# Optimization experiments

Measured on AMD Instinct MI355X. Metric: run time of the kernel, lower is better.

The kernel has to match this reference:

```python
import jax, jax.numpy as jnp
import numpy as np

M_BIT = 8      # BfpConfig.bfp_M_Bit (sign + mantissa bits)
BLOCK = 64     # BFP block size along contraction (K) dim
K_SIZE, STRIDE, PAD = 3, 1, 1


def bfp_quantize(x, m_bit=M_BIT, block=BLOCK):
    """Block-floating-point quantize along last axis: per-block shared exponent
    from max-abs, m_bit-wide signed mantissa, then dequantize back to fp."""
    shape = x.shape
    xb = x.reshape(shape[:-1] + (shape[-1] // block, block))
    maxabs = jnp.max(jnp.abs(xb), axis=-1, keepdims=True)
    exp = jnp.floor(jnp.log2(jnp.maximum(maxabs, jnp.float32(1e-38))))
    scale = jnp.exp2(exp - (m_bit - 2))          # lsb weight for this block
    qmax = jnp.float32(2.0 ** (m_bit - 1) - 1)
    q = jnp.clip(jnp.round(xb / scale), -qmax - 1.0, qmax) * scale
    q = jnp.where(maxabs == 0.0, 0.0, q)
    return q.reshape(shape)


def im2col(x, k, s, p):
    """Torch Unfold ordering: columns flattened as (C, kh, kw). x: [N,C,H,W]."""
    N, C, H, W = x.shape
    Ho = (H + 2 * p - k) // s + 1
    Wo = (W + 2 * p - k) // s + 1
    xp = jnp.pad(x, ((0, 0), (0, 0), (p, p), (p, p)))
    rows = []
    for i in range(k):
        for j in range(k):
            rows.append(xp[:, :, i:i + s * Ho:s, j:j + s * Wo:s])  # [N,C,Ho,Wo]
    # [k*k, N, C, Ho, Wo] -> [N, C, k*k, Ho*Wo] -> [N, C*k*k, Ho*Wo]
    patches = jnp.stack(rows, axis=0).transpose(1, 2, 0, 3, 4)
    return patches.reshape(N, C * k * k, Ho * Wo), Ho, Wo


def setup_inputs() -> dict:
    key = jax.random.key(0)
    k1, k2, k3 = jax.random.split(key, 3)
    inputs = jax.random.normal(k1, (32, 128, 56, 56), dtype=jnp.float32)
    fan_in = 128 * K_SIZE * K_SIZE
    weight = jax.random.normal(k2, (256, 128, K_SIZE, K_SIZE), dtype=jnp.float32) / np.sqrt(fan_in)
    bias = jax.random.normal(k3, (256,), dtype=jnp.float32) * 0.01
    return {"inputs": inputs, "weight": weight, "bias": bias}


def reference(inputs, weight, bias):
    N = inputs.shape[0]
    C_out = weight.shape[0]
    cols, Ho, Wo = im2col(inputs, K_SIZE, STRIDE, PAD)      # [N, K, Ho*Wo]
    a = cols.transpose(0, 2, 1).reshape(-1, cols.shape[1])  # [N*Ho*Wo, K]
    w = weight.reshape(C_out, -1)                           # [C_out, K]
    qa = bfp_quantize(a)
    qw = bfp_quantize(w)
    out = qa @ qw.T + bias                                  # [N*Ho*Wo, C_out]
    out = out.reshape(N, Ho, Wo, C_out).transpose(0, 3, 1, 2)
    return out
```

## Files before the change

### kernel.cpp

```cpp
#include <hip/hip_runtime.h>

typedef short short8 __attribute__((ext_vector_type(8)));
typedef __bf16 bf16x8 __attribute__((ext_vector_type(8)));
typedef float floatx4 __attribute__((ext_vector_type(4)));

__device__ __forceinline__ float make_pow2(int e) {
  return __builtin_bit_cast(float, (unsigned)((e + 127) << 23));
}

typedef __attribute__((address_space(3))) void lds_void;
typedef const __attribute__((address_space(1))) void glob_void;
__device__ __forceinline__ void gload_lds16(const void* g, void* l) {
  __builtin_amdgcn_global_load_lds((glob_void*)g, (lds_void*)l, 16, 0, 0);
}

__global__ void quant_w_kernel(const float* __restrict__ w, unsigned short* __restrict__ qw) {
  int b = blockIdx.x;
  int row = b / 18, kb = b - row * 18;
  int t = threadIdx.x;
  int idx = row * 1152 + kb * 64 + t;
  float v = w[idx];
  float a = fabsf(v);
  #pragma unroll
  for (int off = 32; off; off >>= 1) a = fmaxf(a, __shfl_xor(a, off));
  float q = 0.f;
  if (a > 0.f) {
    int e = (int)((__builtin_bit_cast(unsigned, a) >> 23) & 0xffu) - 127;
    if (e < -126) e = -126;
    float inv = make_pow2(6 - e);
    float s   = make_pow2(e - 6);
    float r = rintf(v * inv);
    r = fminf(fmaxf(r, -128.f), 127.f);
    q = r * s;
  }
  qw[idx] = (unsigned short)(__builtin_bit_cast(unsigned, q) >> 16);
}

__global__ __launch_bounds__(512, 4) void conv_bfp_kernel(
    const float* __restrict__ in, const unsigned short* __restrict__ qw,
    const float* __restrict__ bias, float* __restrict__ out) {
  __shared__ unsigned short As[64 * 64];
  __shared__ unsigned short Bs[2][256 * 64];
  __shared__ float pmax[2][8][64];

  const int bid = blockIdx.x;
  const int mt = (bid & 7) * 196 + (bid >> 3);
  const int t = threadIdx.x;
  const int lane = t & 63;
  const int wave = __builtin_amdgcn_readfirstlane(t >> 6);

  const unsigned m = mt * 64u + lane;
  const unsigned nimg = m / 3136u;
  const unsigned py = m - nimg * 3136u;
  const int y = (int)(py / 56u);
  const int x = (int)(py - (unsigned)y * 56u);
  const int vbase = (int)((nimg * 401408u + (unsigned)y * 56u + (unsigned)x) * 4u);
  int vm = 0;
  #pragma unroll
  for (int i = 0; i < 3; ++i)
    #pragma unroll
    for (int j = 0; j < 3; ++j)
      if ((unsigned)(y + i - 1) < 56u && (unsigned)(x + j - 1) < 56u)
        vm |= 1 << (i * 3 + j);

  const int l3 = lane >> 3, l7 = lane & 7;
  const char* bsrc = (const char*)qw + (size_t)((wave * 32 + l3) * 2304) + ((l7 ^ l3) * 16);

  const int lr = lane & 15;
  const int lk = (lane >> 4) << 4;
  const int swz = (lr & 7) << 4;

  floatx4 acc[4][2] = {};

  auto gather = [&](float (&av)[8], int kb) {
    const int k0 = __builtin_amdgcn_readfirstlane(kb * 64 + wave * 8);
    #pragma unroll
    for (int u = 0; u < 8; ++u) {
      int k = k0 + u;
      int c = (int)((unsigned)k / 9u);
      int ij = k - c * 9;
      int soff = c * 3136 + (ij / 3) * 56 + (ij % 3) - 57;
      const char* pk = (const char*)in + (ptrdiff_t)soff * 4;
      float v = 0.f;
      if ((vm >> ij) & 1)
        v = *(const float*)(pk + vbase);
      av[u] = v;
    }
  };

  auto stage = [&](int kb) {
    char* bdst = (char*)Bs[kb & 1] + wave * 4096;
    #pragma unroll
    for (int c8 = 0; c8 < 4; ++c8)
      gload_lds16(bsrc + (size_t)c8 * 18432 + kb * 128, bdst + c8 * 1024);
  };

  auto lmax_store = [&](float (&av)[8], int kb) {
    float lm = 0.f;
    #pragma unroll
    for (int u = 0; u < 8; ++u) lm = fmaxf(lm, fabsf(av[u]));
    pmax[kb & 1][wave][lane] = lm;
  };

  auto quantWrite = [&](float (&av)[8], int kb) {
    const float* pb = &pmax[kb & 1][0][lane];
    float ma = 0.f;
    #pragma unroll
    for (int j = 0; j < 8; ++j) ma = fmaxf(ma, pb[j * 64]);
    short8 aq;
    if (ma > 0.f) {
      int e = (int)((__builtin_bit_cast(unsigned, ma) >> 23) & 0xffu) - 127;
      if (e < -126) e = -126;
      float inv = make_pow2(6 - e);
      float s   = make_pow2(e - 6);
      #pragma unroll
      for (int u = 0; u < 8; ++u) {
        float r = rintf(av[u] * inv);
        r = fminf(fmaxf(r, -128.f), 127.f);
        float q = r * s;
        aq[u] = (short)(unsigned short)(__builtin_bit_cast(unsigned, q) >> 16);
      }
    } else {
      aq = (short8)0;
    }
    char* arow = (char*)As + lane * 128;
    *(short8*)(arow + ((wave * 16) ^ ((lane & 7) << 4))) = aq;
  };

  float av0[8], av1[8];

  stage(0);
  gather(av0, 0);
  lmax_store(av0, 0);
  __syncthreads();
  quantWrite(av0, 0);
  gather(av1, 1);
  lmax_store(av1, 1);
  __syncthreads();

  auto phase = [&](int kb, float (&avq)[8], float (&avg)[8]) {
    bf16x8 afr[2][4];
    #pragma unroll
    for (int ks = 0; ks < 2; ++ks)
      #pragma unroll
      for (int f = 0; f < 4; ++f)
        afr[ks][f] = __builtin_bit_cast(bf16x8,
            *(const short8*)((const char*)As + (f * 16 + lr) * 128 + ((ks * 64 + lk) ^ swz)));
    __syncthreads();

    if (kb < 17) {
      quantWrite(avq, kb + 1);
      stage(kb + 1);
    }
    if (kb < 16) gather(avg, kb + 2);

    const char* bbase = (const char*)Bs[kb & 1];
    #pragma unroll
    for (int ks = 0; ks < 2; ++ks) {
      const int kbyte = (ks * 64 + lk) ^ swz;
      bf16x8 bfr[2];
      #pragma unroll
      for (int f = 0; f < 2; ++f)
        bfr[f] = __builtin_bit_cast(bf16x8,
            *(const short8*)(bbase + (wave * 32 + f * 16 + lr) * 128 + kbyte));
      #pragma unroll
      for (int fm = 0; fm < 4; ++fm)
        #pragma unroll
        for (int fn = 0; fn < 2; ++fn)
          acc[fm][fn] = __builtin_amdgcn_mfma_f32_16x16x32_bf16(bfr[fn], afr[ks][fm], acc[fm][fn], 0, 0, 0);
    }

    if (kb < 16) lmax_store(avg, kb + 2);
    if (kb < 17) __syncthreads();
  };

  #pragma unroll 1
  for (int kb = 0; kb < 18; kb += 2) {
    phase(kb, av1, av0);
    phase(kb + 1, av0, av1);
  }

  const unsigned ni = (mt * 64u) / 3136u;
  const unsigned pp0 = mt * 64u - ni * 3136u;
  float* obase = out + (size_t)ni * 802816u + pp0;
  const int cg = (lane >> 4) << 2;
  #pragma unroll
  for (int fn = 0; fn < 2; ++fn) {
    floatx4 bv = *(const floatx4*)&bias[wave * 32 + fn * 16 + cg];
    #pragma unroll
    for (int r = 0; r < 4; ++r) {
      int co = wave * 32 + fn * 16 + cg + r;
      float* orow = obase + (size_t)co * 3136u;
      #pragma unroll
      for (int fm = 0; fm < 4; ++fm)
        orow[fm * 16 + lr] = acc[fm][fn][r] + bv[r];
    }
  }
}

extern "C" void kernel_launch(void* const* d_in, const int* in_sizes, int n_in,
                              void* d_out, int out_size, void* d_ws, size_t ws_size,
                              hipStream_t stream) {
  const float* in   = (const float*)d_in[0];
  const float* w    = (const float*)d_in[1];
  const float* bias = (const float*)d_in[2];
  float* out = (float*)d_out;
  unsigned short* qw = (unsigned short*)d_ws;

  quant_w_kernel<<<4608, 64, 0, stream>>>(w, qw);
  conv_bfp_kernel<<<1568, 512, 0, stream>>>(in, qw, bias, out);
}
```

Before: 137.5 us.

## Deepen activation gather pipeline to three stages with explicit waitcnt barriers

Extends the software pipeline so global activation gathers are issued two K-blocks ahead using three rotating register buffers. __syncthreads is replaced with a custom barrier that waits only on LDS counters, and partial vmcnt waits let gathers stay in flight across MFMA blocks. MFMA sections are also raised in wave priority. The aim is to hide global-load latency behind compute, at the cost of more registers, which may lower occupancy, and hand-tuned vmcnt counts that must match the issued loads exactly.

```diff
diff --git a/kernel.cpp b/kernel.cpp
--- a/kernel.cpp
+++ b/kernel.cpp
@@ -12,6 +12,19 @@
 typedef const __attribute__((address_space(1))) void glob_void;
 __device__ __forceinline__ void gload_lds16(const void* g, void* l) {
   __builtin_amdgcn_global_load_lds((glob_void*)g, (lds_void*)l, 16, 0, 0);
+}
+
+__device__ __forceinline__ void barrier_lgkm() {
+  asm volatile("s_waitcnt lgkmcnt(0)" ::: "memory");
+  __builtin_amdgcn_sched_barrier(0);
+  __builtin_amdgcn_s_barrier();
+  asm volatile("" ::: "memory");
+  __builtin_amdgcn_sched_barrier(0);
+}
+
+template <int N> __device__ __forceinline__ void wait_vmcnt() {
+  asm volatile("s_waitcnt vmcnt(%0)" :: "n"(N) : "memory");
+  __builtin_amdgcn_sched_barrier(0);
 }
 
 __global__ void quant_w_kernel(const float* __restrict__ w, unsigned short* __restrict__ qw) {
@@ -127,34 +140,18 @@
     *(short8*)(arow + ((wave * 16) ^ ((lane & 7) << 4))) = aq;
   };
 
-  float av0[8], av1[8];
-
-  stage(0);
-  gather(av0, 0);
-  lmax_store(av0, 0);
-  __syncthreads();
-  quantWrite(av0, 0);
-  gather(av1, 1);
-  lmax_store(av1, 1);
-  __syncthreads();
-
-  auto phase = [&](int kb, float (&avq)[8], float (&avg)[8]) {
-    bf16x8 afr[2][4];
+  auto preloadA = [&](bf16x8 (&afr)[2][4]) {
     #pragma unroll
     for (int ks = 0; ks < 2; ++ks)
       #pragma unroll
       for (int f = 0; f < 4; ++f)
         afr[ks][f] = __builtin_bit_cast(bf16x8,
             *(const short8*)((const char*)As + (f * 16 + lr) * 128 + ((ks * 64 + lk) ^ swz)));
-    __syncthreads();
-
-    if (kb < 17) {
-      quantWrite(avq, kb + 1);
-      stage(kb + 1);
-    }
-    if (kb < 16) gather(avg, kb + 2);
-
+  };
+
+  auto mfmaBlk = [&](bf16x8 (&afr)[2][4], int kb) {
     const char* bbase = (const char*)Bs[kb & 1];
+    __builtin_amdgcn_s_setprio(1);
     #pragma unroll
     for (int ks = 0; ks < 2; ++ks) {
       const int kbyte = (ks * 64 + lk) ^ swz;
@@ -169,15 +166,67 @@
         for (int fn = 0; fn < 2; ++fn)
           acc[fm][fn] = __builtin_amdgcn_mfma_f32_16x16x32_bf16(bfr[fn], afr[ks][fm], acc[fm][fn], 0, 0, 0);
     }
-
-    if (kb < 16) lmax_store(avg, kb + 2);
-    if (kb < 17) __syncthreads();
+    __builtin_amdgcn_s_setprio(0);
+  };
+
+  float avA[8], avB[8], avC[8];
+
+  stage(0);
+  gather(avA, 0);
+  gather(avB, 1);
+  lmax_store(avA, 0);
+  barrier_lgkm();
+  quantWrite(avA, 0);
+  gather(avC, 2);
+  lmax_store(avB, 1);
+  barrier_lgkm();
+
+  auto phase = [&](int kb, float (&q)[8], float (&l)[8], float (&g)[8]) {
+    bf16x8 afr[2][4];
+    preloadA(afr);
+    barrier_lgkm();
+    quantWrite(q, kb + 1);
+    stage(kb + 1);
+    gather(g, kb + 3);
+    wait_vmcnt<20>();
+    mfmaBlk(afr, kb);
+    lmax_store(l, kb + 2);
+    barrier_lgkm();
   };
 
   #pragma unroll 1
-  for (int kb = 0; kb < 18; kb += 2) {
-    phase(kb, av1, av0);
-    phase(kb + 1, av0, av1);
+  for (int kb = 0; kb < 15; kb += 3) {
+    phase(kb,     avB, avC, avA);
+    phase(kb + 1, avC, avA, avB);
+    phase(kb + 2, avA, avB, avC);
+  }
+
+  {
+    bf16x8 afr[2][4];
+    preloadA(afr);
+    barrier_lgkm();
+    quantWrite(avB, 16);
+    stage(16);
+    wait_vmcnt<12>();
+    mfmaBlk(afr, 15);
+    lmax_store(avC, 17);
+    barrier_lgkm();
+  }
+  {
+    bf16x8 afr[2][4];
+    preloadA(afr);
+    barrier_lgkm();
+    quantWrite(avC, 17);
+    stage(17);
+    wait_vmcnt<4>();
+    mfmaBlk(afr, 16);
+    barrier_lgkm();
+  }
+  {
+    bf16x8 afr[2][4];
+    preloadA(afr);
+    wait_vmcnt<0>();
+    mfmaBlk(afr, 17);
   }
 
   const unsigned ni = (mt * 64u) / 3136u;
```

Result: no change. 139.2 us (+1.2%).

## Pre-swizzle quantized weights into MFMA fragment layout and load B directly to registers

Applied to the files above, without the earlier changes.

The weight quantizer now writes bf16 weights in a per-16-channel, per-k-block fragment order so each lane can load its MFMA B operand with one 16-byte global load. This removes the B shared-memory tile and its async global-to-LDS staging. The A tile is double-buffered instead, so each phase needs one barrier rather than two. The MFMA block runs at raised priority with A fragments read from LDS inside the loop. The cost is that B now comes through the global/L2 path into registers, and more registers are held by the double-buffered B fragments.

```diff
diff --git a/kernel.cpp b/kernel.cpp
--- a/kernel.cpp
+++ b/kernel.cpp
@@ -8,39 +8,57 @@
   return __builtin_bit_cast(float, (unsigned)((e + 127) << 23));
 }
 
-typedef __attribute__((address_space(3))) void lds_void;
-typedef const __attribute__((address_space(1))) void glob_void;
-__device__ __forceinline__ void gload_lds16(const void* g, void* l) {
-  __builtin_amdgcn_global_load_lds((glob_void*)g, (lds_void*)l, 16, 0, 0);
+__device__ __forceinline__ void barrier_lgkm() {
+  asm volatile("s_waitcnt lgkmcnt(0)" ::: "memory");
+  __builtin_amdgcn_sched_barrier(0);
+  __builtin_amdgcn_s_barrier();
+  asm volatile("" ::: "memory");
+  __builtin_amdgcn_sched_barrier(0);
 }
 
 __global__ void quant_w_kernel(const float* __restrict__ w, unsigned short* __restrict__ qw) {
   int b = blockIdx.x;
-  int row = b / 18, kb = b - row * 18;
-  int t = threadIdx.x;
-  int idx = row * 1152 + kb * 64 + t;
-  float v = w[idx];
-  float a = fabsf(v);
+  int ct = b / 18, kb = b - ct * 18;
+  int L = threadIdx.x;
+  int co = ct * 16 + (L & 15);
+  int kq = L >> 4;
+  const float* wr = w + co * 1152 + kb * 64 + kq * 8;
+  float v[16];
+  float a = 0.f;
   #pragma unroll
-  for (int off = 32; off; off >>= 1) a = fmaxf(a, __shfl_xor(a, off));
-  float q = 0.f;
+  for (int ks = 0; ks < 2; ++ks)
+    #pragma unroll
+    for (int j = 0; j < 8; ++j) {
+      float t = wr[ks * 32 + j];
+      v[ks * 8 + j] = t;
+      a = fmaxf(a, fabsf(t));
+    }
+  a = fmaxf(a, __shfl_xor(a, 16));
+  a = fmaxf(a, __shfl_xor(a, 32));
+  short8 q0 = (short8)0, q1 = (short8)0;
   if (a > 0.f) {
     int e = (int)((__builtin_bit_cast(unsigned, a) >> 23) & 0xffu) - 127;
     if (e < -126) e = -126;
     float inv = make_pow2(6 - e);
     float s   = make_pow2(e - 6);
-    float r = rintf(v * inv);
-    r = fminf(fmaxf(r, -128.f), 127.f);
-    q = r * s;
+    #pragma unroll
+    for (int u = 0; u < 16; ++u) {
+      float r = rintf(v[u] * inv);
+      r = fminf(fmaxf(r, -128.f), 127.f);
+      float qq = r * s;
+      unsigned short hb = (unsigned short)(__builtin_bit_cast(unsigned, qq) >> 16);
+      if (u < 8) q0[u] = (short)hb; else q1[u - 8] = (short)hb;
+    }
   }
-  qw[idx] = (unsigned short)(__builtin_bit_cast(unsigned, q) >> 16);
+  unsigned short* dst = qw + (size_t)(ct * 18 + kb) * 1024;
+  *(short8*)(dst + L * 8) = q0;
+  *(short8*)(dst + 512 + L * 8) = q1;
 }
 
 __global__ __launch_bounds__(512, 4) void conv_bfp_kernel(
     const float* __restrict__ in, const unsigned short* __restrict__ qw,
     const float* __restrict__ bias, float* __restrict__ out) {
-  __shared__ unsigned short As[64 * 64];
-  __shared__ unsigned short Bs[2][256 * 64];
+  __shared__ unsigned short As[2][64 * 64];
   __shared__ float pmax[2][8][64];
 
   const int bid = blockIdx.x;
@@ -62,9 +80,6 @@
     for (int j = 0; j < 3; ++j)
       if ((unsigned)(y + i - 1) < 56u && (unsigned)(x + j - 1) < 56u)
         vm |= 1 << (i * 3 + j);
-
-  const int l3 = lane >> 3, l7 = lane & 7;
-  const char* bsrc = (const char*)qw + (size_t)((wave * 32 + l3) * 2304) + ((l7 ^ l3) * 16);
 
   const int lr = lane & 15;
   const int lk = (lane >> 4) << 4;
@@ -88,11 +103,15 @@
     }
   };
 
-  auto stage = [&](int kb) {
-    char* bdst = (char*)Bs[kb & 1] + wave * 4096;
-    #pragma unroll
-    for (int c8 = 0; c8 < 4; ++c8)
-      gload_lds16(bsrc + (size_t)c8 * 18432 + kb * 128, bdst + c8 * 1024);
+  auto loadB = [&](bf16x8 (&bq)[2][2], int kb) {
+    #pragma unroll
+    for (int ks = 0; ks < 2; ++ks)
+      #pragma unroll
+      for (int fn = 0; fn < 2; ++fn) {
+        int ct = wave * 2 + fn;
+        bq[ks][fn] = __builtin_bit_cast(bf16x8, *(const short8*)(
+            (const char*)qw + ((size_t)((ct * 18 + kb) * 2 + ks) * 64 + lane) * 16));
+      }
   };
 
   auto lmax_store = [&](float (&av)[8], int kb) {
@@ -123,61 +142,53 @@
     } else {
       aq = (short8)0;
     }
-    char* arow = (char*)As + lane * 128;
+    char* arow = (char*)As[kb & 1] + lane * 128;
     *(short8*)(arow + ((wave * 16) ^ ((lane & 7) << 4))) = aq;
   };
 
-  float av0[8], av1[8];
-
-  stage(0);
-  gather(av0, 0);
-  lmax_store(av0, 0);
-  __syncthreads();
-  quantWrite(av0, 0);
-  gather(av1, 1);
-  lmax_store(av1, 1);
-  __syncthreads();
-
-  auto phase = [&](int kb, float (&avq)[8], float (&avg)[8]) {
-    bf16x8 afr[2][4];
-    #pragma unroll
-    for (int ks = 0; ks < 2; ++ks)
-      #pragma unroll
-      for (int f = 0; f < 4; ++f)
-        afr[ks][f] = __builtin_bit_cast(bf16x8,
-            *(const short8*)((const char*)As + (f * 16 + lr) * 128 + ((ks * 64 + lk) ^ swz)));
-    __syncthreads();
-
-    if (kb < 17) {
-      quantWrite(avq, kb + 1);
-      stage(kb + 1);
-    }
-    if (kb < 16) gather(avg, kb + 2);
-
-    const char* bbase = (const char*)Bs[kb & 1];
+  auto mfmaBlk = [&](bf16x8 (&bq)[2][2], int kb) {
+    const char* abase = (const char*)As[kb & 1];
+    __builtin_amdgcn_s_setprio(1);
     #pragma unroll
     for (int ks = 0; ks < 2; ++ks) {
       const int kbyte = (ks * 64 + lk) ^ swz;
-      bf16x8 bfr[2];
-      #pragma unroll
-      for (int f = 0; f < 2; ++f)
-        bfr[f] = __builtin_bit_cast(bf16x8,
-            *(const short8*)(bbase + (wave * 32 + f * 16 + lr) * 128 + kbyte));
-      #pragma unroll
-      for (int fm = 0; fm < 4; ++fm)
+      #pragma unroll
+      for (int fm = 0; fm < 4; ++fm) {
+        bf16x8 af = __builtin_bit_cast(bf16x8,
+            *(const short8*)(abase + (fm * 16 + lr) * 128 + kbyte));
         #pragma unroll
         for (int fn = 0; fn < 2; ++fn)
-          acc[fm][fn] = __builtin_amdgcn_mfma_f32_16x16x32_bf16(bfr[fn], afr[ks][fm], acc[fm][fn], 0, 0, 0);
-    }
-
+          acc[fm][fn] = __builtin_amdgcn_mfma_f32_16x16x32_bf16(bq[ks][fn], af, acc[fm][fn], 0, 0, 0);
+      }
+    }
+    __builtin_amdgcn_s_setprio(0);
+  };
+
+  float av0[8], av1[8];
+  bf16x8 bqA[2][2], bqB[2][2];
+
+  gather(av0, 0);
+  loadB(bqA, 0);
+  gather(av1, 1);
+  lmax_store(av0, 0);
+  lmax_store(av1, 1);
+  barrier_lgkm();
+  quantWrite(av0, 0);
+
+  auto phase = [&](int kb, float (&avq)[8], float (&avg)[8],
+                   bf16x8 (&bqc)[2][2], bf16x8 (&bqn)[2][2]) {
+    barrier_lgkm();
+    if (kb < 17) quantWrite(avq, kb + 1);
+    if (kb < 16) gather(avg, kb + 2);
+    if (kb < 17) loadB(bqn, kb + 1);
+    mfmaBlk(bqc, kb);
     if (kb < 16) lmax_store(avg, kb + 2);
-    if (kb < 17) __syncthreads();
   };
 
   #pragma unroll 1
   for (int kb = 0; kb < 18; kb += 2) {
-    phase(kb, av1, av0);
-    phase(kb + 1, av0, av1);
+    phase(kb,     av1, av0, bqA, bqB);
+    phase(kb + 1, av0, av1, bqB, bqA);
   }
 
   const unsigned ni = (mt * 64u) / 3136u;
@@ -207,6 +218,6 @@
   float* out = (float*)d_out;
   unsigned short* qw = (unsigned short*)d_ws;
 
-  quant_w_kernel<<<4608, 64, 0, stream>>>(w, qw);
+  quant_w_kernel<<<288, 64, 0, stream>>>(w, qw);
   conv_bfp_kernel<<<1568, 512, 0, stream>>>(in, qw, bias, out);
 }
```

Result: faster. 130.6 us (-5.0%).
